# Kernel optimization log

Measured on AMD Instinct MI355X. Metric: run time of the kernel, lower is better.

## Reference

```python
import jax, jax.numpy as jnp
import numpy as np

K = 3  # torch_geometric knn_interpolate default
EPS = 1e-16


def knn_interpolate(l_y, l_pos, h_pos):
    # squared distances [N_h, N_l]
    d2 = jnp.sum((h_pos[:, None, :] - l_pos[None, :, :]) ** 2, axis=-1)
    neg_d, idx = jax.lax.top_k(-d2, K)          # k nearest: idx [N_h, K]
    w = 1.0 / jnp.maximum(-neg_d, EPS)           # inverse squared-distance weights
    feats = l_y[idx]                             # [N_h, K, F] gather
    return jnp.sum(w[..., None] * feats, axis=1) / jnp.sum(w, axis=1, keepdims=True)


def mlp(x, W1, b1, W2, b2, W3, b3):
    x = jax.nn.relu(x @ W1 + b1)
    x = jax.nn.relu(x @ W2 + b2)
    return x @ W3 + b3


def setup_inputs() -> dict:
    key = jax.random.key(0)
    ks = jax.random.split(key, 8)
    N_h, N_l, H, O = 32768, 8192, 512, 128
    s1 = 1.0 / np.sqrt(H)
    return {
        "emb": jax.random.normal(ks[0], (N_h, H), jnp.float32),
        "l_y": jax.random.normal(ks[1], (N_l, O), jnp.float32),
        "l_pos": jax.random.uniform(ks[2], (N_l, 3), jnp.float32),
        "h_pos": jax.random.uniform(ks[3], (N_h, 3), jnp.float32),
        "W1": jax.random.normal(ks[4], (H, H), jnp.float32) * s1,
        "b1": jnp.zeros((H,), jnp.float32),
        "W2": jax.random.normal(ks[5], (H, H), jnp.float32) * s1,
        "b2": jnp.zeros((H,), jnp.float32),
        "W3": jax.random.normal(ks[6], (H, O), jnp.float32) * s1,
        "b3": jnp.zeros((O,), jnp.float32),
    }


def reference(emb, l_y, l_pos, h_pos, W1, b1, W2, b2, W3, b3):
    x = mlp(emb, W1, b1, W2, b2, W3, b3)
    return x + knn_interpolate(l_y, l_pos, h_pos)
```

## Files before the change

kernel.cpp:

```cpp
#include <hip/hip_runtime.h>
#include <stdint.h>

typedef __attribute__((ext_vector_type(4))) float f32x4;
typedef __attribute__((ext_vector_type(8))) short bf16x8;
typedef __attribute__((ext_vector_type(4))) unsigned short u16x4;

#define AS1(p) ((const __attribute__((address_space(1))) void*)(p))
#define AS3(p) ((__attribute__((address_space(3))) void*)(p))

__device__ __forceinline__ unsigned short f2bf(float f){
  unsigned u = __builtin_bit_cast(unsigned, f);
  u += 0x7FFF + ((u >> 16) & 1);
  return (unsigned short)(u >> 16);
}

template<int N> __device__ __forceinline__ void waitcnt_vm(){
  if constexpr (N==0) asm volatile("s_waitcnt vmcnt(0)" ::: "memory");
  else if constexpr (N==4) asm volatile("s_waitcnt vmcnt(4)" ::: "memory");
  else if constexpr (N==5) asm volatile("s_waitcnt vmcnt(5)" ::: "memory");
  else if constexpr (N==8) asm volatile("s_waitcnt vmcnt(8)" ::: "memory");
}

__global__ __launch_bounds__(256) void k_transpose_cast(const float* __restrict__ in,
                                                        unsigned short* __restrict__ out,
                                                        int R, int C){
  __shared__ float tile[32][33];
  int tx = threadIdx.x & 31, ty = threadIdx.x >> 5;
  int c0 = blockIdx.x*32, r0 = blockIdx.y*32;
  #pragma unroll
  for (int i = 0; i < 4; i++)
    tile[ty + i*8][tx] = in[(size_t)(r0 + ty + i*8)*C + c0 + tx];
  __syncthreads();
  #pragma unroll
  for (int i = 0; i < 4; i++)
    out[(size_t)(c0 + ty + i*8)*R + r0 + tx] = f2bf(tile[tx][ty + i*8]);
}

template<int NC, int TW, int MINW, bool AF32, bool RELU, bool OUTBF16>
__global__ __launch_bounds__(TW, MINW) void k_gemm(const void* __restrict__ Av,
                                                   const unsigned short* __restrict__ Bt,
                                                   const float* __restrict__ bias,
                                                   void* __restrict__ out, int K){
  constexpr int WARPS_N = TW/128;
  constexpr int WN = NC/WARPS_N;
  constexpr int NI = WN/16;
  constexpr int IA = AF32 ? 0 : (128*4)/TW;
  constexpr int IB = (NC*4)/TW;
  constexpr int LS = IA + IB;

  __shared__ short As[3][128*32];
  __shared__ short Bs[3][NC*32];

  const int tid  = threadIdx.x;
  const int lane = tid & 63, wid = tid >> 6;
  const int wr = wid / WARPS_N, wc = wid % WARPS_N;
  const int l15 = lane & 15, lk = lane >> 4;
  const int bm = blockIdx.x;

  const unsigned short* Bsrc[IB];
  #pragma unroll
  for (int q = 0; q < IB; q++){
    int row = q*(TW/4) + (tid >> 2);
    int ch  = (tid & 3) ^ ((row >> 1) & 3);
    Bsrc[q] = Bt + (size_t)row*K + ch*8;
  }
  const unsigned short* Asrc16[IA > 0 ? IA : 1];
  if constexpr (!AF32){
    #pragma unroll
    for (int a = 0; a < IA; a++){
      int row = a*(TW/4) + (tid >> 2);
      int ch  = (tid & 3) ^ ((row >> 1) & 3);
      Asrc16[a] = (const unsigned short*)Av + (size_t)bm*128*K + (size_t)row*K + ch*8;
    }
  }
  const float* A32 = (const float*)Av + (size_t)bm*128*K + (size_t)(tid>>2)*K + (size_t)(tid&3)*8;
  const int wch = ((tid & 3) ^ (((tid >> 2) >> 1) & 3));
  const int woff = (tid >> 2)*32 + wch*8;

#define STAGE_B(t_, bb_) do{ int k0_ = (t_) << 5; _Pragma("unroll") \
  for (int q = 0; q < IB; q++) \
    __builtin_amdgcn_global_load_lds(AS1(Bsrc[q] + k0_), AS3(&Bs[bb_][(q*(TW/4))*32 + tid*8]), 16, 0, 0); \
}while(0)
#define STAGE_A16(t_, bb_) do{ int k0_ = (t_) << 5; _Pragma("unroll") \
  for (int a = 0; a < IA; a++) \
    __builtin_amdgcn_global_load_lds(AS1(Asrc16[a] + k0_), AS3(&As[bb_][(a*(TW/4))*32 + tid*8]), 16, 0, 0); \
}while(0)
#define A_CONV_WRITE(bb_) do{ bf16x8 p_; _Pragma("unroll") \
  for (int j_ = 0; j_ < 4; j_++){ p_[j_] = (short)f2bf(ra0[j_]); p_[j_+4] = (short)f2bf(ra1[j_]); } \
  *(bf16x8*)&As[bb_][woff] = p_; \
}while(0)

  f32x4 acc[4][NI];
  #pragma unroll
  for (int i = 0; i < 4; i++)
    #pragma unroll
    for (int j = 0; j < NI; j++) acc[i][j] = (f32x4){0.f,0.f,0.f,0.f};

  const int nt = K >> 5;
  f32x4 ra0, ra1;

  if constexpr (AF32){
    ra0 = *(const f32x4*)(A32);
    ra1 = *(const f32x4*)(A32 + 4);
    STAGE_B(0, 0);
    STAGE_B(1, 1);
    waitcnt_vm<8>();
    A_CONV_WRITE(0);
    waitcnt_vm<4>();
  } else {
    STAGE_A16(0, 0); STAGE_B(0, 0);
    STAGE_A16(1, 1); STAGE_B(1, 1);
  }

  int b = 0;
  for (int t = 0; t < nt; ++t){
    if constexpr (!AF32){
      if (t + 1 < nt) waitcnt_vm<LS>(); else waitcnt_vm<0>();
    }
    asm volatile("s_waitcnt lgkmcnt(0)" ::: "memory");
    __builtin_amdgcn_s_barrier();
    __builtin_amdgcn_sched_barrier(0);

    int nb = b + 2; if (nb >= 3) nb -= 3;
    if constexpr (AF32){
      if (t + 1 < nt){
        int k1 = (t + 1) << 5;
        ra0 = *(const f32x4*)(A32 + k1);
        ra1 = *(const f32x4*)(A32 + k1 + 4);
      }
      if (t + 2 < nt) STAGE_B(t + 2, nb);
    } else {
      if (t + 2 < nt){ STAGE_A16(t + 2, nb); STAGE_B(t + 2, nb); }
    }

    bf16x8 af[4], bg[NI];
    #pragma unroll
    for (int i = 0; i < 4; i++){
      int R = wr*64 + i*16 + l15;
      af[i] = *(const bf16x8*)&As[b][R*32 + (lk ^ ((R >> 1) & 3))*8];
    }
    #pragma unroll
    for (int j = 0; j < NI; j++){
      int R = wc*WN + j*16 + l15;
      bg[j] = *(const bf16x8*)&Bs[b][R*32 + (lk ^ ((R >> 1) & 3))*8];
    }
    #pragma unroll
    for (int i = 0; i < 4; i++)
      #pragma unroll
      for (int j = 0; j < NI; j++)
        acc[i][j] = __builtin_amdgcn_mfma_f32_16x16x32_bf16(af[i], bg[j], acc[i][j], 0, 0, 0);

    if constexpr (AF32){
      if (t + 1 < nt){
        if (t + 2 < nt) waitcnt_vm<4>(); else waitcnt_vm<0>();
        int wb = b + 1; if (wb >= 3) wb -= 3;
        A_CONV_WRITE(wb);
      }
    }
    b = (b + 1 == 3) ? 0 : b + 1;
  }
#undef STAGE_B
#undef STAGE_A16
#undef A_CONV_WRITE

  const int row0 = bm*128 + wr*64 + lk*4;
  const int col0 = wc*WN + l15;
  #pragma unroll
  for (int i = 0; i < 4; i++){
    #pragma unroll
    for (int j = 0; j < NI; j++){
      int col = col0 + j*16;
      float bv = bias[col];
      #pragma unroll
      for (int r = 0; r < 4; r++){
        int row = row0 + i*16 + r;
        float v = acc[i][j][r] + bv;
        if (RELU) v = fmaxf(v, 0.f);
        if (OUTBF16) ((unsigned short*)out)[(size_t)row*NC + col] = f2bf(v);
        else         ((float*)out)[(size_t)row*NC + col] = v;
      }
    }
  }
}

#define GD 14
#define GD3 (GD*GD*GD)
#define NL 8192

__device__ __forceinline__ int cellcoord(float x){
  int c = (int)(x * (float)GD);
  return min(GD-1, max(0, c));
}

__global__ __launch_bounds__(64) void k_zero(int* __restrict__ p){
  #pragma unroll
  for (int i = 0; i < 16; i++)
    ((int4*)p)[threadIdx.x*16 + i] = (int4){0,0,0,0};
}

__global__ __launch_bounds__(256) void k_hist(const float* __restrict__ l_pos,
                                              int* __restrict__ hist){
  int i = blockIdx.x*256 + threadIdx.x;
  float x = l_pos[3*i], y = l_pos[3*i+1], z = l_pos[3*i+2];
  int c = (cellcoord(z)*GD + cellcoord(y))*GD + cellcoord(x);
  atomicAdd(&hist[c], 1);
}

__global__ __launch_bounds__(1024) void k_scan(const int* __restrict__ hist,
                                               int* __restrict__ cellStart,
                                               int* __restrict__ cursor){
  __shared__ int s[1024];
  int t = threadIdx.x;
  int4 v = ((const int4*)hist)[t];
  int sum = v.x + v.y + v.z + v.w;
  s[t] = sum;
  __syncthreads();
  for (int off = 1; off < 1024; off <<= 1){
    int val = (t >= off) ? s[t-off] : 0;
    __syncthreads();
    s[t] += val;
    __syncthreads();
  }
  int base = s[t] - sum;
  int4 cs;
  cs.x = base;
  cs.y = base + v.x;
  cs.z = base + v.x + v.y;
  cs.w = base + v.x + v.y + v.z;
  ((int4*)cellStart)[t] = cs;
  ((int4*)cursor)[t]    = cs;
}

__global__ __launch_bounds__(256) void k_scatter(const float* __restrict__ l_pos,
                                                 int* __restrict__ cursor,
                                                 float4* __restrict__ sorted){
  int i = blockIdx.x*256 + threadIdx.x;
  float x = l_pos[3*i], y = l_pos[3*i+1], z = l_pos[3*i+2];
  int c = (cellcoord(z)*GD + cellcoord(y))*GD + cellcoord(x);
  int slot = atomicAdd(&cursor[c], 1);
  float4 q; q.x = x; q.y = y; q.z = z; q.w = __int_as_float(i);
  sorted[slot] = q;
}

#define KNN_INS(dv, gi) \
  if (gi != i0 && gi != i1 && gi != i2 && \
      (dv < d2 || (dv == d2 && gi < i2))){ \
    if (dv < d1 || (dv == d1 && gi < i1)){ \
      d2 = d1; i2 = i1; \
      if (dv < d0 || (dv == d0 && gi < i0)){ d1 = d0; i1 = i0; d0 = dv; i0 = gi; } \
      else { d1 = dv; i1 = gi; } \
    } else { d2 = dv; i2 = gi; } \
  }

#define KNN_MERGE16() \
  _Pragma("unroll") \
  for (int m = 1; m < 16; m <<= 1){ \
    float e0 = __shfl_xor(d0, m), e1 = __shfl_xor(d1, m), e2 = __shfl_xor(d2, m); \
    int   j0 = __shfl_xor(i0, m), j1 = __shfl_xor(i1, m), j2 = __shfl_xor(i2, m); \
    KNN_INS(e0, j0); KNN_INS(e1, j1); KNN_INS(e2, j2); \
  }

__global__ __launch_bounds__(256) void k_knn_grid(const float* __restrict__ h_pos,
                                                  const int* __restrict__ cellStart,
                                                  const float4* __restrict__ sorted,
                                                  float* __restrict__ w,
                                                  int* __restrict__ idx){
  const int t = blockIdx.x*256 + threadIdx.x;
  const int h = t >> 4, sl = t & 15;
  const float hx = h_pos[3*h], hy = h_pos[3*h+1], hz = h_pos[3*h+2];
  const int cx = cellcoord(hx), cy = cellcoord(hy), cz = cellcoord(hz);
  const float cs = 1.0f/(float)GD;
  float d0 = 3e38f, d1 = 3e38f, d2 = 3e38f;
  int   i0 = 0x7fffffff, i1 = 0x7fffffff, i2 = 0x7fffffff;

  for (int ci = sl; ci < 27; ci += 16){
    int dz = ci/9 - 1, dy = (ci - (ci/9)*9)/3 - 1, dx = ci % 3 - 1;
    int zz = cz+dz, yy = cy+dy, xx = cx+dx;
    if ((unsigned)zz >= GD || (unsigned)yy >= GD || (unsigned)xx >= GD) continue;
    int c = (zz*GD + yy)*GD + xx;
    int p0 = cellStart[c], p1 = cellStart[c+1];
    for (int p = p0; p < p1; p++){
      float4 qq = sorted[p];
      float ddx = hx - qq.x, ddy = hy - qq.y, ddz = hz - qq.z;
      float d = fmaf(ddx, ddx, fmaf(ddy, ddy, ddz*ddz));
      int gi = __float_as_int(qq.w);
      KNN_INS(d, gi);
    }
  }
  KNN_MERGE16();

  for (int r = 2; r < GD; r++){
    int rp = r - 1;
    float B = 3e38f;
    if (cx - rp > 0)      B = fminf(B, hx - (float)(cx-rp)*cs);
    if (cx + rp + 1 < GD) B = fminf(B, (float)(cx+rp+1)*cs - hx);
    if (cy - rp > 0)      B = fminf(B, hy - (float)(cy-rp)*cs);
    if (cy + rp + 1 < GD) B = fminf(B, (float)(cy+rp+1)*cs - hy);
    if (cz - rp > 0)      B = fminf(B, hz - (float)(cz-rp)*cs);
    if (cz + rp + 1 < GD) B = fminf(B, (float)(cz+rp+1)*cs - hz);
    if (d2 <= B*B) break;

    int side = 2*r + 1, ss = side*side, tot = ss*side;
    for (int ci = sl; ci < tot; ci += 16){
      int dz = ci/ss - r;
      int rem = ci - (ci/ss)*ss;
      int dy = rem/side - r, dx = rem - (rem/side)*side - r;
      int adx = abs(dx), ady = abs(dy), adz = abs(dz);
      if (max(adx, max(ady, adz)) < r) continue;
      int zz = cz+dz, yy = cy+dy, xx = cx+dx;
      if ((unsigned)zz >= GD || (unsigned)yy >= GD || (unsigned)xx >= GD) continue;
      int c = (zz*GD + yy)*GD + xx;
      int p0 = cellStart[c], p1 = cellStart[c+1];
      for (int p = p0; p < p1; p++){
        float4 qq = sorted[p];
        float ddx = hx - qq.x, ddy = hy - qq.y, ddz = hz - qq.z;
        float d = fmaf(ddx, ddx, fmaf(ddy, ddy, ddz*ddz));
        int gi = __float_as_int(qq.w);
        KNN_INS(d, gi);
      }
    }
    KNN_MERGE16();
  }

  if (sl == 0){
    w[3*h+0] = 1.0f/fmaxf(d0, 1e-16f); idx[3*h+0] = i0;
    w[3*h+1] = 1.0f/fmaxf(d1, 1e-16f); idx[3*h+1] = i1;
    w[3*h+2] = 1.0f/fmaxf(d2, 1e-16f); idx[3*h+2] = i2;
  }
}

__global__ __launch_bounds__(256) void k_knn_gather(const float* __restrict__ w,
                                                    const int* __restrict__ idx,
                                                    const float* __restrict__ l_y,
                                                    float* __restrict__ out){
  const int t = blockIdx.x*256 + threadIdx.x;
  const int h = t >> 5, lane = t & 31;
  const float w0 = w[h*3+0], w1 = w[h*3+1], w2 = w[h*3+2];
  const int   j0 = idx[h*3+0], j1 = idx[h*3+1], j2 = idx[h*3+2];
  const f32x4* ly4 = (const f32x4*)l_y;
  f32x4 a = ly4[(size_t)j0*32 + lane]*w0
          + ly4[(size_t)j1*32 + lane]*w1
          + ly4[(size_t)j2*32 + lane]*w2;
  float inv = 1.0f/(w0 + w1 + w2);
  f32x4* o4 = (f32x4*)out;
  size_t oi = (size_t)h*32 + lane;
  o4[oi] = o4[oi] + a*inv;
}

extern "C" void kernel_launch(void* const* d_in, const int* in_sizes, int n_in,
                              void* d_out, int out_size, void* d_ws, size_t ws_size,
                              hipStream_t stream){
  const float* emb   = (const float*)d_in[0];
  const float* l_y   = (const float*)d_in[1];
  const float* l_pos = (const float*)d_in[2];
  const float* h_pos = (const float*)d_in[3];
  const float* W1    = (const float*)d_in[4];
  const float* b1    = (const float*)d_in[5];
  const float* W2    = (const float*)d_in[6];
  const float* b2    = (const float*)d_in[7];
  const float* W3    = (const float*)d_in[8];
  const float* b3    = (const float*)d_in[9];

  const int M = 32768, H = 512, O = 128;

  char* ws = (char*)d_ws;
  unsigned short* bufA = (unsigned short*)(ws);
  unsigned short* bufB = (unsigned short*)(ws + 33554432);
  unsigned short* W1t  = (unsigned short*)(ws + 67108864);
  unsigned short* W2t  = (unsigned short*)(ws + 67633152);
  unsigned short* W3t  = (unsigned short*)(ws + 68157440);
  int*    hist      = (int*)   (ws + 68288512);
  int*    cellStart = (int*)   (ws + 68304896);
  int*    cursor    = (int*)   (ws + 68321280);
  float4* sorted    = (float4*)(ws + 68354048);
  float* wts = (float*)(ws + 74579968);
  int*   idx = (int*)  (ws + 74973184);

  k_transpose_cast<<<dim3(H/32, H/32), 256, 0, stream>>>(W1, W1t, H, H);
  k_transpose_cast<<<dim3(H/32, H/32), 256, 0, stream>>>(W2, W2t, H, H);
  k_transpose_cast<<<dim3(O/32, H/32), 256, 0, stream>>>(W3, W3t, H, O);

  k_gemm<512, 512, 2, true,  true,  true ><<<dim3(M/128), 512, 0, stream>>>(emb,  W1t, b1, bufB, H);
  k_gemm<512, 512, 2, false, true,  true ><<<dim3(M/128), 512, 0, stream>>>(bufB, W2t, b2, bufA, H);
  k_gemm<128, 256, 3, false, false, false><<<dim3(M/128), 256, 0, stream>>>(bufA, W3t, b3, d_out, H);

  k_zero<<<dim3(1), 64, 0, stream>>>(hist);
  k_hist<<<dim3(NL/256), 256, 0, stream>>>(l_pos, hist);
  k_scan<<<dim3(1), 1024, 0, stream>>>(hist, cellStart, cursor);
  k_scatter<<<dim3(NL/256), 256, 0, stream>>>(l_pos, cursor, sorted);
  k_knn_grid<<<dim3(M*16/256), 256, 0, stream>>>(h_pos, cellStart, sorted, wts, idx);
  k_knn_gather<<<dim3(M*32/256), 256, 0, stream>>>(wts, idx, l_y, (float*)d_out);
}
```

Before: 139.5 us.

## Merge weight transposes, reorder KNN before MLP, restructure GEMM loop barriers

The three weight transpose/cast launches become one kernel indexed by blockIdx.z. The KNN pipeline now runs first and writes the interpolation directly to the output, and the final GEMM adds its result into that output instead of the gather doing a read-modify-write. Inside the GEMM main loop, the LDS fragment loads move ahead of issuing the next prefetch, the wait and barrier move to the end of each iteration, and s_setprio raises priority around the MFMA block. Occupancy for the last GEMM changes from 3 to 2 waves per SIMD, and the extra read of the output in the GEMM epilogue adds memory traffic.

```diff
diff --git a/kernel.cpp b/kernel.cpp
--- a/kernel.cpp
+++ b/kernel.cpp
@@ -16,14 +16,23 @@
 
 template<int N> __device__ __forceinline__ void waitcnt_vm(){
   if constexpr (N==0) asm volatile("s_waitcnt vmcnt(0)" ::: "memory");
+  else if constexpr (N==2) asm volatile("s_waitcnt vmcnt(2)" ::: "memory");
   else if constexpr (N==4) asm volatile("s_waitcnt vmcnt(4)" ::: "memory");
   else if constexpr (N==5) asm volatile("s_waitcnt vmcnt(5)" ::: "memory");
-  else if constexpr (N==8) asm volatile("s_waitcnt vmcnt(8)" ::: "memory");
-}
-
-__global__ __launch_bounds__(256) void k_transpose_cast(const float* __restrict__ in,
-                                                        unsigned short* __restrict__ out,
-                                                        int R, int C){
+  else if constexpr (N==6) asm volatile("s_waitcnt vmcnt(6)" ::: "memory");
+}
+
+__global__ __launch_bounds__(256) void k_transpose3(const float* __restrict__ W1,
+                                                    const float* __restrict__ W2,
+                                                    const float* __restrict__ W3,
+                                                    unsigned short* __restrict__ W1t,
+                                                    unsigned short* __restrict__ W2t,
+                                                    unsigned short* __restrict__ W3t){
+  const int z = blockIdx.z;
+  const float* in; unsigned short* out; int R, C;
+  if (z == 0){ in = W1; out = W1t; R = 512; C = 512; }
+  else if (z == 1){ in = W2; out = W2t; R = 512; C = 512; }
+  else { in = W3; out = W3t; R = 512; C = 128; if (blockIdx.x >= 4) return; }
   __shared__ float tile[32][33];
   int tx = threadIdx.x & 31, ty = threadIdx.x >> 5;
   int c0 = blockIdx.x*32, r0 = blockIdx.y*32;
@@ -36,11 +45,11 @@
     out[(size_t)(c0 + ty + i*8)*R + r0 + tx] = f2bf(tile[tx][ty + i*8]);
 }
 
-template<int NC, int TW, int MINW, bool AF32, bool RELU, bool OUTBF16>
-__global__ __launch_bounds__(TW, MINW) void k_gemm(const void* __restrict__ Av,
-                                                   const unsigned short* __restrict__ Bt,
-                                                   const float* __restrict__ bias,
-                                                   void* __restrict__ out, int K){
+template<int NC, int TW, bool AF32, bool RELU, bool OUTBF16, bool ADDOUT>
+__global__ __launch_bounds__(TW, 2) void k_gemm(const void* __restrict__ Av,
+                                                const unsigned short* __restrict__ Bt,
+                                                const float* __restrict__ bias,
+                                                void* __restrict__ out, int K){
   constexpr int WARPS_N = TW/128;
   constexpr int WN = NC/WARPS_N;
   constexpr int NI = WN/16;
@@ -74,8 +83,7 @@
     }
   }
   const float* A32 = (const float*)Av + (size_t)bm*128*K + (size_t)(tid>>2)*K + (size_t)(tid&3)*8;
-  const int wch = ((tid & 3) ^ (((tid >> 2) >> 1) & 3));
-  const int woff = (tid >> 2)*32 + wch*8;
+  const int woff = (tid >> 2)*32 + ((tid & 3) ^ (((tid >> 2) >> 1) & 3))*8;
 
 #define STAGE_B(t_, bb_) do{ int k0_ = (t_) << 5; _Pragma("unroll") \
   for (int q = 0; q < IB; q++) \
@@ -104,59 +112,60 @@
     ra1 = *(const f32x4*)(A32 + 4);
     STAGE_B(0, 0);
     STAGE_B(1, 1);
-    waitcnt_vm<8>();
+    waitcnt_vm<4>();
     A_CONV_WRITE(0);
-    waitcnt_vm<4>();
+    asm volatile("s_waitcnt lgkmcnt(0)" ::: "memory");
   } else {
     STAGE_A16(0, 0); STAGE_B(0, 0);
     STAGE_A16(1, 1); STAGE_B(1, 1);
-  }
+    waitcnt_vm<LS>();
+  }
+  __builtin_amdgcn_s_barrier();
 
   int b = 0;
   for (int t = 0; t < nt; ++t){
-    if constexpr (!AF32){
-      if (t + 1 < nt) waitcnt_vm<LS>(); else waitcnt_vm<0>();
-    }
-    asm volatile("s_waitcnt lgkmcnt(0)" ::: "memory");
-    __builtin_amdgcn_s_barrier();
-    __builtin_amdgcn_sched_barrier(0);
-
-    int nb = b + 2; if (nb >= 3) nb -= 3;
+    bf16x8 af[4], bg[NI];
+    #pragma unroll
+    for (int i = 0; i < 4; i++){
+      int R = wr*64 + i*16 + l15;
+      af[i] = *(const bf16x8*)&As[b][R*32 + (lk ^ ((R >> 1) & 3))*8];
+    }
+    #pragma unroll
+    for (int j = 0; j < NI; j++){
+      int R = wc*WN + j*16 + l15;
+      bg[j] = *(const bf16x8*)&Bs[b][R*32 + (lk ^ ((R >> 1) & 3))*8];
+    }
+
+    int b2 = b + 2; if (b2 >= 3) b2 -= 3;
     if constexpr (AF32){
       if (t + 1 < nt){
         int k1 = (t + 1) << 5;
         ra0 = *(const f32x4*)(A32 + k1);
         ra1 = *(const f32x4*)(A32 + k1 + 4);
       }
-      if (t + 2 < nt) STAGE_B(t + 2, nb);
+      if (t + 2 < nt) STAGE_B(t + 2, b2);
     } else {
-      if (t + 2 < nt){ STAGE_A16(t + 2, nb); STAGE_B(t + 2, nb); }
-    }
-
-    bf16x8 af[4], bg[NI];
-    #pragma unroll
-    for (int i = 0; i < 4; i++){
-      int R = wr*64 + i*16 + l15;
-      af[i] = *(const bf16x8*)&As[b][R*32 + (lk ^ ((R >> 1) & 3))*8];
-    }
-    #pragma unroll
-    for (int j = 0; j < NI; j++){
-      int R = wc*WN + j*16 + l15;
-      bg[j] = *(const bf16x8*)&Bs[b][R*32 + (lk ^ ((R >> 1) & 3))*8];
-    }
+      if (t + 2 < nt){ STAGE_A16(t + 2, b2); STAGE_B(t + 2, b2); }
+    }
+
+    __builtin_amdgcn_s_setprio(1);
     #pragma unroll
     for (int i = 0; i < 4; i++)
       #pragma unroll
       for (int j = 0; j < NI; j++)
         acc[i][j] = __builtin_amdgcn_mfma_f32_16x16x32_bf16(af[i], bg[j], acc[i][j], 0, 0, 0);
-
+    __builtin_amdgcn_s_setprio(0);
+
+    if (t + 2 < nt) waitcnt_vm<(AF32 ? 4 : LS)>();
+    else            waitcnt_vm<0>();
     if constexpr (AF32){
       if (t + 1 < nt){
-        if (t + 2 < nt) waitcnt_vm<4>(); else waitcnt_vm<0>();
         int wb = b + 1; if (wb >= 3) wb -= 3;
         A_CONV_WRITE(wb);
       }
     }
+    asm volatile("s_waitcnt lgkmcnt(0)" ::: "memory");
+    __builtin_amdgcn_s_barrier();
     b = (b + 1 == 3) ? 0 : b + 1;
   }
 #undef STAGE_B
@@ -176,6 +185,7 @@
         int row = row0 + i*16 + r;
         float v = acc[i][j][r] + bv;
         if (RELU) v = fmaxf(v, 0.f);
+        if (ADDOUT) v = v + ((const float*)out)[(size_t)row*NC + col];
         if (OUTBF16) ((unsigned short*)out)[(size_t)row*NC + col] = f2bf(v);
         else         ((float*)out)[(size_t)row*NC + col] = v;
       }
@@ -342,9 +352,7 @@
           + ly4[(size_t)j1*32 + lane]*w1
           + ly4[(size_t)j2*32 + lane]*w2;
   float inv = 1.0f/(w0 + w1 + w2);
-  f32x4* o4 = (f32x4*)out;
-  size_t oi = (size_t)h*32 + lane;
-  o4[oi] = o4[oi] + a*inv;
+  ((f32x4*)out)[(size_t)h*32 + lane] = a*inv;
 }
 
 extern "C" void kernel_launch(void* const* d_in, const int* in_sizes, int n_in,
@@ -361,7 +369,7 @@
   const float* W3    = (const float*)d_in[8];
   const float* b3    = (const float*)d_in[9];
 
-  const int M = 32768, H = 512, O = 128;
+  const int M = 32768, H = 512;
 
   char* ws = (char*)d_ws;
   unsigned short* bufA = (unsigned short*)(ws);
@@ -376,13 +384,7 @@
   float* wts = (float*)(ws + 74579968);
   int*   idx = (int*)  (ws + 74973184);
 
-  k_transpose_cast<<<dim3(H/32, H/32), 256, 0, stream>>>(W1, W1t, H, H);
-  k_transpose_cast<<<dim3(H/32, H/32), 256, 0, stream>>>(W2, W2t, H, H);
-  k_transpose_cast<<<dim3(O/32, H/32), 256, 0, stream>>>(W3, W3t, H, O);
-
-  k_gemm<512, 512, 2, true,  true,  true ><<<dim3(M/128), 512, 0, stream>>>(emb,  W1t, b1, bufB, H);
-  k_gemm<512, 512, 2, false, true,  true ><<<dim3(M/128), 512, 0, stream>>>(bufB, W2t, b2, bufA, H);
-  k_gemm<128, 256, 3, false, false, false><<<dim3(M/128), 256, 0, stream>>>(bufA, W3t, b3, d_out, H);
+  k_transpose3<<<dim3(16, 16, 3), 256, 0, stream>>>(W1, W2, W3, W1t, W2t, W3t);
 
   k_zero<<<dim3(1), 64, 0, stream>>>(hist);
   k_hist<<<dim3(NL/256), 256, 0, stream>>>(l_pos, hist);
@@ -390,4 +392,8 @@
   k_scatter<<<dim3(NL/256), 256, 0, stream>>>(l_pos, cursor, sorted);
   k_knn_grid<<<dim3(M*16/256), 256, 0, stream>>>(h_pos, cellStart, sorted, wts, idx);
   k_knn_gather<<<dim3(M*32/256), 256, 0, stream>>>(wts, idx, l_y, (float*)d_out);
-}
+
+  k_gemm<512, 512, true,  true,  true,  false><<<dim3(M/128), 512, 0, stream>>>(emb,  W1t, b1, bufB, H);
+  k_gemm<512, 512, false, true,  true,  false><<<dim3(M/128), 512, 0, stream>>>(bufB, W2t, b2, bufA, H);
+  k_gemm<128, 256, false, false, false, true ><<<dim3(M/128), 256, 0, stream>>>(bufA, W3t, b3, d_out, H);
+}
```

Result: faster. 122.9 us (-11.9%).
